# Kernel optimization log

Measured on AMD Instinct MI355X. Metric: run time of the kernel, lower is better.

Reference implementation:

```python
import jax, jax.numpy as jnp
import numpy as np

B, S, D = 2, 2048, 1024
H, HD = 16, 64

def setup_inputs() -> dict:
    key = jax.random.key(0)
    k1, k2, k3, k4 = jax.random.split(key, 4)
    inputs = jax.random.normal(k1, (B, S, D), dtype=jnp.float32)
    scale = 1.0 / np.sqrt(D)
    Wq = jax.random.normal(k2, (D, H * HD), dtype=jnp.float32) * scale
    Wk = jax.random.normal(k3, (D, H * HD), dtype=jnp.float32) * scale
    Wv = jax.random.normal(k4, (D, H * HD), dtype=jnp.float32) * scale
    return {"inputs": inputs, "Wq": Wq, "Wk": Wk, "Wv": Wv}

def _split_heads(x):
    # [B,S,H*HD] -> [B,H,S,HD]; tf.split along last axis == reshape then transpose
    b, s, _ = x.shape
    return x.reshape(b, s, H, HD).transpose(0, 2, 1, 3)

def reference(inputs, Wq, Wk, Wv):
    q = _split_heads(inputs @ Wq)  # [B,H,S,HD]
    k = _split_heads(inputs @ Wk)
    v = _split_heads(inputs @ Wv)
    scores = jnp.einsum("bhsd,bhtd->bhst", q, k) / jnp.sqrt(jnp.float32(HD))
    attn = jax.nn.softmax(scores, axis=-1)  # [B,H,S,S]
    out = jnp.einsum("bhst,bhtd->bhsd", attn, v)  # [B,H,S,HD]
    # concat heads back: [B,S,H*HD]
    return out.transpose(0, 2, 1, 3).reshape(inputs.shape[0], inputs.shape[1], H * HD)
```

## Files before the change

kernel.cpp:

```cpp
#include <hip/hip_runtime.h>
#include <hip/hip_fp16.h>

typedef __attribute__((ext_vector_type(8))) short short8;
typedef __attribute__((ext_vector_type(4))) float f32x4;
typedef __attribute__((ext_vector_type(16))) float f32x16;

#define B_  2
#define S_  2048
#define D_  1024
#define H_  16
#define HD_ 64
#define M_  (B_*S_)
#define N_  (H_*HD_)
#define HSZ ((size_t)B_*H_*S_*HD_)
#define BHS_ (B_*H_*S_)

#define QSCALE 0.18033688011112042f
#define M0 8.0f

__device__ __forceinline__ unsigned short f2bf(float f) {
  unsigned int u = __float_as_uint(f);
  u += 0x7fffu + ((u >> 16) & 1u);
  return (unsigned short)(u >> 16);
}

__device__ __forceinline__ unsigned int cvt_pk_bf16(float lo, float hi) {
  unsigned int r;
  asm("v_cvt_pk_bf16_f32 %0, %1, %2" : "=v"(r) : "v"(lo), "v"(hi));
  return r;
}

__device__ __forceinline__ float exp2_fast(float x) {
  float r;
  asm("v_exp_f32 %0, %1" : "=v"(r) : "v"(x));
  return r;
}

__device__ __forceinline__ void gll16(const void* g, void* l) {
  __builtin_amdgcn_global_load_lds(
      (const __attribute__((address_space(1))) void*)g,
      (__attribute__((address_space(3))) void*)l, 16, 0, 0);
}

__global__ __launch_bounds__(256) void cvt_all_kernel(const float* __restrict__ x,
                                                      const float* __restrict__ w0,
                                                      const float* __restrict__ w1,
                                                      const float* __restrict__ w2,
                                                      unsigned short* __restrict__ xb,
                                                      unsigned short* __restrict__ wt) {
  __shared__ float tile[32][33];
  int bid = blockIdx.x;
  if (bid < 4096) {
    int i = bid * 256 + threadIdx.x;
    float4 v = reinterpret_cast<const float4*>(x)[i];
    ushort4 o;
    o.x = f2bf(v.x); o.y = f2bf(v.y); o.z = f2bf(v.z); o.w = f2bf(v.w);
    reinterpret_cast<ushort4*>(xb)[i] = o;
    return;
  }
  int wid = bid - 4096;
  int z = wid >> 10, rem = wid & 1023;
  int nbase = (rem & 31) * 32, kbase = (rem >> 5) * 32;
  int tx = threadIdx.x & 31, ty = threadIdx.x >> 5;
  const float* w = z == 0 ? w0 : (z == 1 ? w1 : w2);
  unsigned short* o = wt + (size_t)z * D_ * N_;
#pragma unroll
  for (int i = 0; i < 4; i++)
    tile[ty + i*8][tx] = w[(size_t)(kbase + ty + i*8) * N_ + nbase + tx];
  __syncthreads();
#pragma unroll
  for (int i = 0; i < 4; i++)
    o[(size_t)(nbase + ty + i*8) * D_ + kbase + tx] = f2bf(tile[tx][ty + i*8]);
}

__global__ __launch_bounds__(256) void qkv_gemm_kernel(const unsigned short* __restrict__ xb,
                                                       const unsigned short* __restrict__ wt,
                                                       unsigned short* __restrict__ qkv) {
  __shared__ __align__(16) unsigned short As[128 * 64];
  __shared__ __align__(16) unsigned short Bs[128 * 64];
  const unsigned short* w = wt + (size_t)blockIdx.z * D_ * N_;
  unsigned short* out = qkv + (size_t)blockIdx.z * HSZ;
  int lane = threadIdx.x & 63, wave = threadIdx.x >> 6;
  int lr = lane & 15, lk = lane >> 4;
  int mblk = blockIdx.y * 128, nblk = blockIdx.x * 128;
  int wm = (wave >> 1) * 64, wn = (wave & 1) * 64;

  int srow0 = wave * 32 + (lane >> 3);
  int scol = lane & 7;
  f32x4 acc[4][4] = {};

  for (int kk = 0; kk < D_; kk += 64) {
    __syncthreads();
#pragma unroll
    for (int it = 0; it < 4; it++) {
      int row = srow0 + it * 8;
      int ce = (scol ^ (row & 7)) * 8;
      gll16(xb + (size_t)(mblk + row) * D_ + kk + ce,
            (void*)(As + (size_t)(wave * 4 + it) * 512));
      gll16(w  + (size_t)(nblk + row) * D_ + kk + ce,
            (void*)(Bs + (size_t)(wave * 4 + it) * 512));
    }
    __syncthreads();

    short8 a[2][4], b[2][4];
#pragma unroll
    for (int i = 0; i < 4; i++) {
      int row = wm + i * 16 + lr;
      const char* rp = (const char*)As + row * 128;
#pragma unroll
      for (int ks = 0; ks < 2; ks++)
        a[ks][i] = *reinterpret_cast<const short8*>(rp + ((((ks*4 + lk) ^ (row & 7))) << 4));
    }
#pragma unroll
    for (int j = 0; j < 4; j++) {
      int row = wn + j * 16 + lr;
      const char* rp = (const char*)Bs + row * 128;
#pragma unroll
      for (int ks = 0; ks < 2; ks++)
        b[ks][j] = *reinterpret_cast<const short8*>(rp + ((((ks*4 + lk) ^ (row & 7))) << 4));
    }
#pragma unroll
    for (int ks = 0; ks < 2; ks++)
#pragma unroll
      for (int i = 0; i < 4; i++)
#pragma unroll
        for (int j = 0; j < 4; j++)
          acc[i][j] = __builtin_amdgcn_mfma_f32_16x16x32_bf16(a[ks][i], b[ks][j], acc[i][j], 0, 0, 0);
  }

  if (blockIdx.z == 2) {
#pragma unroll
    for (int i = 0; i < 4; i++) {
      int m0 = mblk + wm + i*16 + lk*4;
      int bb = m0 >> 11, s0 = m0 & (S_-1);
#pragma unroll
      for (int j = 0; j < 4; j++) {
        int n = nblk + wn + j*16 + lr;
        int h = n >> 6, d = n & (HD_-1);
        ushort4 pk;
        pk.x = f2bf(acc[i][j][0]); pk.y = f2bf(acc[i][j][1]);
        pk.z = f2bf(acc[i][j][2]); pk.w = f2bf(acc[i][j][3]);
        *reinterpret_cast<ushort4*>(out + ((size_t)(bb*H_ + h)*HD_ + d)*S_ + s0) = pk;
      }
    }
  } else {
    float qs = (blockIdx.z == 0) ? QSCALE : 1.0f;
#pragma unroll
    for (int i = 0; i < 4; i++)
#pragma unroll
      for (int j = 0; j < 4; j++)
#pragma unroll
        for (int r = 0; r < 4; r++) {
          int m = mblk + wm + i*16 + lk*4 + r;
          int n = nblk + wn + j*16 + lr;
          int bb = m >> 11, s = m & (S_-1), h = n >> 6, d = n & (HD_-1);
          out[(((size_t)bb * H_ + h) * S_ + s) * HD_ + d] = f2bf(acc[i][j][r] * qs);
        }
  }
}

__global__ __launch_bounds__(256, 2) void attn_kernel(const unsigned short* __restrict__ qkv,
                                                      __half* __restrict__ Opart,
                                                      float* __restrict__ L) {
  int hid = blockIdx.x;
  int wrk = (hid & 7) * 64 + (hid >> 3);
  int bh = wrk >> 4, qt2 = (wrk >> 1) & 7, half = wrk & 1;

  const unsigned short* Q  = qkv +            (size_t)bh * S_ * HD_;
  const unsigned short* K  = qkv + HSZ   +    (size_t)bh * S_ * HD_;
  const unsigned short* Vt = qkv + 2*HSZ +    (size_t)bh * HD_ * S_;
  int lane = threadIdx.x & 63, wave = threadIdx.x >> 6;
  int ql = lane & 31, hi = lane >> 5;
  int qbase = qt2 * 256 + wave * 64;
  int tid = threadIdx.x;
  int kv0 = half * (S_/2);

  __shared__ __align__(16) unsigned short Ks[4][64 * 64];
  __shared__ __align__(16) unsigned short Vs[4][64 * 64];

#define STAGE(b, kc) do {                                                        \
    _Pragma("unroll")                                                            \
    for (int it = 0; it < 2; it++) {                                             \
      int ci = it * 256 + tid;                                                   \
      int rr = ci >> 3, cc = ci & 7;                                             \
      int ce = (cc ^ (rr & 7) ^ ((rr >> 3) & 7)) * 8;                            \
      gll16(K  + (size_t)((kc) + rr) * HD_ + ce, (void*)(Ks[b] + (size_t)ci*8)); \
      gll16(Vt + (size_t)rr * S_ + (kc) + ce,    (void*)(Vs[b] + (size_t)ci*8)); \
    }                                                                            \
  } while (0)

  short8 qf[2][4];
#pragma unroll
  for (int qt = 0; qt < 2; qt++)
#pragma unroll
    for (int ds = 0; ds < 4; ds++)
      qf[qt][ds] = *reinterpret_cast<const short8*>(
          Q + (size_t)(qbase + qt*32 + ql) * HD_ + ds*16 + hi*8);

  f32x16 oacc[2][2] = {};
  float lsum0 = 0.f, lsum1 = 0.f;

  STAGE(0, kv0);
  STAGE(1, kv0 + 64);

#pragma unroll 4
  for (int kt = 0; kt < 16; kt++) {
    int buf = kt & 3;
    if ((kt & 1) == 0) {
      __syncthreads();
      if (kt < 14) {
        STAGE((kt + 2) & 3, kv0 + (kt + 2) * 64);
        STAGE((kt + 3) & 3, kv0 + (kt + 3) * 64);
      }
    }

    short8 kf[2][4];
#pragma unroll
    for (int kh = 0; kh < 2; kh++) {
      int row = kh*32 + ql;
      const char* rp = (const char*)Ks[buf] + row * 128;
      int sw = (row & 7) ^ ((row >> 3) & 7);
#pragma unroll
      for (int ds = 0; ds < 4; ds++)
        kf[kh][ds] = *reinterpret_cast<const short8*>(rp + (((ds*2 + hi) ^ sw) << 4));
    }
    f32x16 s0[2], s1[2];
#pragma unroll
    for (int kh = 0; kh < 2; kh++)
#pragma unroll
      for (int r = 0; r < 16; r++) { s0[kh][r] = -M0; s1[kh][r] = -M0; }
    __builtin_amdgcn_s_setprio(1);
#pragma unroll
    for (int kh = 0; kh < 2; kh++)
#pragma unroll
      for (int ds = 0; ds < 4; ds++) {
        s0[kh] = __builtin_amdgcn_mfma_f32_32x32x16_bf16(kf[kh][ds], qf[0][ds], s0[kh], 0, 0, 0);
        s1[kh] = __builtin_amdgcn_mfma_f32_32x32x16_bf16(kf[kh][ds], qf[1][ds], s1[kh], 0, 0, 0);
      }
    __builtin_amdgcn_s_setprio(0);

#pragma unroll
    for (int kh = 0; kh < 2; kh++)
#pragma unroll
      for (int r = 0; r < 16; r++) {
        s0[kh][r] = exp2_fast(s0[kh][r]);
        s1[kh][r] = exp2_fast(s1[kh][r]);
      }
    {
      float ts[8];
#pragma unroll
      for (int r = 0; r < 8; r++)
        ts[r] = (s0[0][r] + s0[0][r+8]) + (s0[1][r] + s0[1][r+8]);
#pragma unroll
      for (int st = 4; st > 0; st >>= 1)
#pragma unroll
        for (int r = 0; r < st; r++) ts[r] += ts[r + st];
      lsum0 += ts[0] + __shfl_xor(ts[0], 32);
    }
    {
      float ts[8];
#pragma unroll
      for (int r = 0; r < 8; r++)
        ts[r] = (s1[0][r] + s1[0][r+8]) + (s1[1][r] + s1[1][r+8]);
#pragma unroll
      for (int st = 4; st > 0; st >>= 1)
#pragma unroll
        for (int r = 0; r < st; r++) ts[r] += ts[r + st];
      lsum1 += ts[0] + __shfl_xor(ts[0], 32);
    }

    short8 vf[4][2];
#pragma unroll
    for (int ks = 0; ks < 4; ks++) {
      int o = (ks & 1) * 8;
      int kh = ks >> 1;
      unsigned int w0 = cvt_pk_bf16(s0[kh][o+0], s0[kh][o+1]);
      unsigned int w1 = cvt_pk_bf16(s0[kh][o+2], s0[kh][o+3]);
      unsigned int w2 = cvt_pk_bf16(s0[kh][o+4], s0[kh][o+5]);
      unsigned int w3 = cvt_pk_bf16(s0[kh][o+6], s0[kh][o+7]);
      asm("v_permlane32_swap_b32 %0, %1" : "+v"(w0), "+v"(w2));
      asm("v_permlane32_swap_b32 %0, %1" : "+v"(w1), "+v"(w3));
      union { unsigned int u[4]; short8 v; } pf;
      pf.u[0] = w0; pf.u[1] = w1; pf.u[2] = w2; pf.u[3] = w3;
      __builtin_amdgcn_s_setprio(1);
#pragma unroll
      for (int dh = 0; dh < 2; dh++) {
        int row = dh*32 + ql;
        int sw = (row & 7) ^ ((row >> 3) & 7);
        vf[ks][dh] = *reinterpret_cast<const short8*>(
            (const char*)Vs[buf] + row * 128 + (((ks*2 + hi) ^ sw) << 4));
        oacc[0][dh] = __builtin_amdgcn_mfma_f32_32x32x16_bf16(vf[ks][dh], pf.v, oacc[0][dh], 0, 0, 0);
      }
      __builtin_amdgcn_s_setprio(0);
    }
#pragma unroll
    for (int ks = 0; ks < 4; ks++) {
      int o = (ks & 1) * 8;
      int kh = ks >> 1;
      unsigned int w0 = cvt_pk_bf16(s1[kh][o+0], s1[kh][o+1]);
      unsigned int w1 = cvt_pk_bf16(s1[kh][o+2], s1[kh][o+3]);
      unsigned int w2 = cvt_pk_bf16(s1[kh][o+4], s1[kh][o+5]);
      unsigned int w3 = cvt_pk_bf16(s1[kh][o+6], s1[kh][o+7]);
      asm("v_permlane32_swap_b32 %0, %1" : "+v"(w0), "+v"(w2));
      asm("v_permlane32_swap_b32 %0, %1" : "+v"(w1), "+v"(w3));
      union { unsigned int u[4]; short8 v; } pf;
      pf.u[0] = w0; pf.u[1] = w1; pf.u[2] = w2; pf.u[3] = w3;
      __builtin_amdgcn_s_setprio(1);
#pragma unroll
      for (int dh = 0; dh < 2; dh++)
        oacc[1][dh] = __builtin_amdgcn_mfma_f32_32x32x16_bf16(vf[ks][dh], pf.v, oacc[1][dh], 0, 0, 0);
      __builtin_amdgcn_s_setprio(0);
    }
  }

#pragma unroll
  for (int qt = 0; qt < 2; qt++) {
    int s = qbase + qt*32 + ql;
    size_t prow = (size_t)half * BHS_ + (size_t)bh * S_ + s;
    __half* orow = Opart + prow * HD_;
#pragma unroll
    for (int dh = 0; dh < 2; dh++)
#pragma unroll
      for (int a = 0; a < 4; a++) {
        union { __half2 h[2]; uint2 u; } pk;
        pk.h[0] = __float22half2_rn(make_float2(oacc[qt][dh][a*4+0], oacc[qt][dh][a*4+1]));
        pk.h[1] = __float22half2_rn(make_float2(oacc[qt][dh][a*4+2], oacc[qt][dh][a*4+3]));
        *reinterpret_cast<uint2*>(orow + dh*32 + 8*a + 4*hi) = pk.u;
      }
    if (hi == 0) L[prow] = (qt == 0) ? lsum0 : lsum1;
  }
#undef STAGE
}

__global__ __launch_bounds__(256) void combine_kernel(const __half* __restrict__ Opart,
                                                      const float* __restrict__ L,
                                                      float* __restrict__ out) {
  int idx = blockIdx.x * 256 + threadIdx.x;
  int row = idx >> 3;
  int dc = (idx & 7) * 8;
  float inv = 1.0f / (L[row] + L[BHS_ + row]);
  const __half2* p0 = reinterpret_cast<const __half2*>(Opart + (size_t)row * HD_ + dc);
  const __half2* p1 = reinterpret_cast<const __half2*>(Opart + ((size_t)BHS_ + row) * HD_ + dc);
  float r[8];
#pragma unroll
  for (int i = 0; i < 4; i++) {
    float2 a = __half22float2(p0[i]);
    float2 b = __half22float2(p1[i]);
    r[2*i+0] = (a.x + b.x) * inv;
    r[2*i+1] = (a.y + b.y) * inv;
  }
  int bh = row >> 11, s = row & (S_-1);
  int b = bh >> 4, h = bh & (H_-1);
  float* po = out + ((size_t)b * S_ + s) * N_ + h * HD_ + dc;
  float4 v0; v0.x = r[0]; v0.y = r[1]; v0.z = r[2]; v0.w = r[3];
  float4 v1; v1.x = r[4]; v1.y = r[5]; v1.z = r[6]; v1.w = r[7];
  *reinterpret_cast<float4*>(po)     = v0;
  *reinterpret_cast<float4*>(po + 4) = v1;
}

extern "C" void kernel_launch(void* const* d_in, const int* in_sizes, int n_in,
                              void* d_out, int out_size, void* d_ws, size_t ws_size,
                              hipStream_t stream) {
  const float* X  = (const float*)d_in[0];
  const float* Wq = (const float*)d_in[1];
  const float* Wk = (const float*)d_in[2];
  const float* Wv = (const float*)d_in[3];
  float* out = (float*)d_out;

  unsigned short* Xb  = (unsigned short*)d_ws;
  unsigned short* Wt  = Xb + (size_t)M_ * D_;
  unsigned short* QKV = Wt + (size_t)3 * D_ * N_;
  __half* Opart = (__half*)(QKV + 3 * HSZ);
  float* L    = (float*)(Opart + (size_t)2 * BHS_ * HD_);

  cvt_all_kernel<<<4096 + 3072, 256, 0, stream>>>(X, Wq, Wk, Wv, Xb, Wt);
  qkv_gemm_kernel<<<dim3(N_/128, M_/128, 3), 256, 0, stream>>>(Xb, Wt, QKV);
  attn_kernel<<<(S_/256) * (B_*H_) * 2, 256, 0, stream>>>(QKV, Opart, L);
  combine_kernel<<<(BHS_*8)/256, 256, 0, stream>>>(Opart, L, out);
}
```

Measured before the change: 112.0 us.

## Double-buffer QKV GEMM LDS, remap blocks across XCDs, vectorize Q/K stores

The QKV projection GEMM now double-buffers its LDS tiles, issuing the global-to-LDS loads for the next K-slice before computing the current one. That removes one barrier per iteration and overlaps load latency with MFMA work. The 3D grid becomes a 1D grid with an XCD-aware index remap, so neighbouring tiles land on the same chiplet for L2 reuse. For Q and K the MFMA operands are swapped so each lane holds four consecutive head-dim values, which lets the epilogue write 8-byte vector stores instead of scalar ones. The cost is double the LDS footprint, which can lower occupancy.

Measured after the change: 107.6 us (median of 4 runs). 3.9% less time.

```diff
diff --git a/kernel.cpp b/kernel.cpp
--- a/kernel.cpp
+++ b/kernel.cpp
@@ -73,40 +73,49 @@
     o[(size_t)(nbase + ty + i*8) * D_ + kbase + tx] = f2bf(tile[tx][ty + i*8]);
 }
 
-__global__ __launch_bounds__(256) void qkv_gemm_kernel(const unsigned short* __restrict__ xb,
+__global__ __launch_bounds__(256) void qkv_gemm_kernel(const unsigned short* __restrict__ xbp,
                                                        const unsigned short* __restrict__ wt,
                                                        unsigned short* __restrict__ qkv) {
-  __shared__ __align__(16) unsigned short As[128 * 64];
-  __shared__ __align__(16) unsigned short Bs[128 * 64];
-  const unsigned short* w = wt + (size_t)blockIdx.z * D_ * N_;
-  unsigned short* out = qkv + (size_t)blockIdx.z * HSZ;
+  __shared__ __align__(16) unsigned short As[2][128 * 64];
+  __shared__ __align__(16) unsigned short Bs[2][128 * 64];
+  int hid = blockIdx.x;
+  int wq = (hid & 7) * 96 + (hid >> 3);
+  int z = wq >> 8, gy = (wq >> 3) & 31, gx = wq & 7;
+  const unsigned short* w = wt + (size_t)z * D_ * N_;
+  unsigned short* out = qkv + (size_t)z * HSZ;
   int lane = threadIdx.x & 63, wave = threadIdx.x >> 6;
   int lr = lane & 15, lk = lane >> 4;
-  int mblk = blockIdx.y * 128, nblk = blockIdx.x * 128;
+  int mblk = gy * 128, nblk = gx * 128;
   int wm = (wave >> 1) * 64, wn = (wave & 1) * 64;
 
   int srow0 = wave * 32 + (lane >> 3);
   int scol = lane & 7;
   f32x4 acc[4][4] = {};
 
-  for (int kk = 0; kk < D_; kk += 64) {
+#define STAGE_G(b, kk) do {                                                      \
+    _Pragma("unroll")                                                            \
+    for (int it = 0; it < 4; it++) {                                             \
+      int row = srow0 + it * 8;                                                  \
+      int ce = (scol ^ (row & 7)) * 8;                                           \
+      gll16(xbp + (size_t)(mblk + row) * D_ + (kk) + ce,                         \
+            (void*)(As[b] + (size_t)(wave * 4 + it) * 512));                     \
+      gll16(w   + (size_t)(nblk + row) * D_ + (kk) + ce,                         \
+            (void*)(Bs[b] + (size_t)(wave * 4 + it) * 512));                     \
+    }                                                                            \
+  } while (0)
+
+  STAGE_G(0, 0);
+
+  for (int kt = 0; kt < 16; kt++) {
+    int bufg = kt & 1;
     __syncthreads();
-#pragma unroll
-    for (int it = 0; it < 4; it++) {
-      int row = srow0 + it * 8;
-      int ce = (scol ^ (row & 7)) * 8;
-      gll16(xb + (size_t)(mblk + row) * D_ + kk + ce,
-            (void*)(As + (size_t)(wave * 4 + it) * 512));
-      gll16(w  + (size_t)(nblk + row) * D_ + kk + ce,
-            (void*)(Bs + (size_t)(wave * 4 + it) * 512));
-    }
-    __syncthreads();
+    if (kt < 15) STAGE_G(bufg ^ 1, (kt + 1) * 64);
 
     short8 a[2][4], b[2][4];
 #pragma unroll
     for (int i = 0; i < 4; i++) {
       int row = wm + i * 16 + lr;
-      const char* rp = (const char*)As + row * 128;
+      const char* rp = (const char*)As[bufg] + row * 128;
 #pragma unroll
       for (int ks = 0; ks < 2; ks++)
         a[ks][i] = *reinterpret_cast<const short8*>(rp + ((((ks*4 + lk) ^ (row & 7))) << 4));
@@ -114,21 +123,32 @@
 #pragma unroll
     for (int j = 0; j < 4; j++) {
       int row = wn + j * 16 + lr;
-      const char* rp = (const char*)Bs + row * 128;
+      const char* rp = (const char*)Bs[bufg] + row * 128;
 #pragma unroll
       for (int ks = 0; ks < 2; ks++)
         b[ks][j] = *reinterpret_cast<const short8*>(rp + ((((ks*4 + lk) ^ (row & 7))) << 4));
     }
-#pragma unroll
-    for (int ks = 0; ks < 2; ks++)
-#pragma unroll
-      for (int i = 0; i < 4; i++)
-#pragma unroll
-        for (int j = 0; j < 4; j++)
-          acc[i][j] = __builtin_amdgcn_mfma_f32_16x16x32_bf16(a[ks][i], b[ks][j], acc[i][j], 0, 0, 0);
-  }
-
-  if (blockIdx.z == 2) {
+    if (z == 2) {
+#pragma unroll
+      for (int ks = 0; ks < 2; ks++)
+#pragma unroll
+        for (int i = 0; i < 4; i++)
+#pragma unroll
+          for (int j = 0; j < 4; j++)
+            acc[i][j] = __builtin_amdgcn_mfma_f32_16x16x32_bf16(a[ks][i], b[ks][j], acc[i][j], 0, 0, 0);
+    } else {
+#pragma unroll
+      for (int ks = 0; ks < 2; ks++)
+#pragma unroll
+        for (int i = 0; i < 4; i++)
+#pragma unroll
+          for (int j = 0; j < 4; j++)
+            acc[i][j] = __builtin_amdgcn_mfma_f32_16x16x32_bf16(b[ks][j], a[ks][i], acc[i][j], 0, 0, 0);
+    }
+  }
+#undef STAGE_G
+
+  if (z == 2) {
 #pragma unroll
     for (int i = 0; i < 4; i++) {
       int m0 = mblk + wm + i*16 + lk*4;
@@ -144,18 +164,22 @@
       }
     }
   } else {
-    float qs = (blockIdx.z == 0) ? QSCALE : 1.0f;
-#pragma unroll
-    for (int i = 0; i < 4; i++)
-#pragma unroll
-      for (int j = 0; j < 4; j++)
-#pragma unroll
-        for (int r = 0; r < 4; r++) {
-          int m = mblk + wm + i*16 + lk*4 + r;
-          int n = nblk + wn + j*16 + lr;
-          int bb = m >> 11, s = m & (S_-1), h = n >> 6, d = n & (HD_-1);
-          out[(((size_t)bb * H_ + h) * S_ + s) * HD_ + d] = f2bf(acc[i][j][r] * qs);
-        }
+    float qs = (z == 0) ? QSCALE : 1.0f;
+#pragma unroll
+    for (int i = 0; i < 4; i++) {
+      int m = mblk + wm + i*16 + lr;
+      int bb = m >> 11, s = m & (S_-1);
+      unsigned short* ob = out + (size_t)bb*H_*S_*HD_ + (size_t)s*HD_;
+#pragma unroll
+      for (int j = 0; j < 4; j++) {
+        int n0 = nblk + wn + j*16 + lk*4;
+        int h = n0 >> 6, d = n0 & (HD_-1);
+        ushort4 pk;
+        pk.x = f2bf(acc[i][j][0]*qs); pk.y = f2bf(acc[i][j][1]*qs);
+        pk.z = f2bf(acc[i][j][2]*qs); pk.w = f2bf(acc[i][j][3]*qs);
+        *reinterpret_cast<ushort4*>(ob + (size_t)h*S_*HD_ + d) = pk;
+      }
+    }
   }
 }
 
@@ -374,7 +398,7 @@
   float* L    = (float*)(Opart + (size_t)2 * BHS_ * HD_);
 
   cvt_all_kernel<<<4096 + 3072, 256, 0, stream>>>(X, Wq, Wk, Wv, Xb, Wt);
-  qkv_gemm_kernel<<<dim3(N_/128, M_/128, 3), 256, 0, stream>>>(Xb, Wt, QKV);
+  qkv_gemm_kernel<<<768, 256, 0, stream>>>(Xb, Wt, QKV);
   attn_kernel<<<(S_/256) * (B_*H_) * 2, 256, 0, stream>>>(QKV, Opart, L);
   combine_kernel<<<(BHS_*8)/256, 256, 0, stream>>>(Opart, L, out);
 }
```
